# Kernel optimization log

Hardware: AMD Instinct MI355X
Metric: run time of the kernel (lower is better)

Reference implementation:

```python
import jax, jax.numpy as jnp
import numpy as np

B, N, FIN = 64, 128, 768
NFEAT, NHID, NHEADS, NCLASS = 1024, 512, 8, 512
ALPHA = 0.2
NEG_E = -9e15
NEG_S = -9e10


def setup_inputs():
    rng = np.random.RandomState(0)
    x = rng.randn(B, N, FIN).astype(np.float32)
    offset_mapping = np.zeros((B, N, 2), dtype=np.int32)
    attention_mask = np.zeros((B, N), dtype=np.float32)
    tag = np.zeros((B, N), dtype=np.float32)
    for b in range(B):
        pos, k, groups = 1, 0, 0
        n_words = int(rng.randint(30, 60))
        for _ in range(n_words):
            wl = int(rng.randint(1, 4))
            if k + wl > 120:
                break
            for _t in range(wl):
                offset_mapping[b, k] = (pos, pos + 2)  # contiguous inside word
                pos += 2
                k += 1
            pos += 1  # 1-char gap => word boundary: end == next_start - 1
            groups += 1
        groups -= 1  # last word is never closed (matches torch loop semantics)
        attention_mask[b, :groups] = 1.0
        tag[b, :groups] = (rng.rand(groups) > 0.1).astype(np.float32)
        tag[b, 0] = 1.0
    adj = (rng.rand(B, N, N) < 0.3).astype(np.float32)
    adj = np.clip(adj + np.eye(N, dtype=np.float32)[None], 0.0, 1.0)
    s = 0.02
    p = {
        'Wg_w': s * rng.randn(FIN, NFEAT), 'Wg_b': np.zeros(NFEAT),
        'hW_w': s * rng.randn(NHEADS, NFEAT, NHID), 'hW_b': np.zeros((NHEADS, NHID)),
        'ha_w': s * rng.randn(NHEADS, 2 * NHID), 'ha_b': np.zeros(NHEADS),
        'oW_w': s * rng.randn(NHID * NHEADS, NCLASS), 'oW_b': np.zeros(NCLASS),
        'oa_w': s * rng.randn(2 * NCLASS), 'oa_b': np.zeros(()),
        'fin_w': s * rng.randn(NCLASS, 1), 'fin_b': np.zeros(1),
    }
    inp = {
        'x': jnp.asarray(x), 'tag': jnp.asarray(tag),
        'offset_mapping': jnp.asarray(offset_mapping),
        'attention_mask': jnp.asarray(attention_mask), 'adj': jnp.asarray(adj),
    }
    for kk, vv in p.items():
        inp[kk] = jnp.asarray(np.asarray(vv, dtype=np.float32))
    return inp


def _group_pool(x, offs):
    # Vectorized form of the offset-grouped mean pooling loop.
    zero = (offs[:, :, 0] == 0) & (offs[:, :, 1] == 0)  # padding rows
    fz = jnp.argmax(zero, axis=1)                       # first padding row (break)
    pos = jnp.arange(N)
    valid = pos[None, :] < fz[:, None]
    nxt_start = jnp.concatenate([offs[:, 1:, 0], jnp.zeros((offs.shape[0], 1), offs.dtype)], axis=1)
    boundary = valid & (offs[:, :, 1] == nxt_start - 1)
    bi = boundary.astype(jnp.int32)
    cs = jnp.cumsum(bi, axis=1)
    seg = cs - bi                 # exclusive cumsum: group id per token
    G = cs[:, -1]                 # number of closed groups per row

    def per(xb, segb, bb):
        sums = jax.ops.segment_sum(xb, segb, num_segments=N + 1)[:N]
        cnts = jax.ops.segment_sum(jnp.ones((N,), xb.dtype), segb, num_segments=N + 1)[:N]
        ends = jax.ops.segment_sum((jnp.arange(N) + 1) * bb, segb, num_segments=N + 1)[:N]
        return sums, cnts, ends

    sums, cnts, ends = jax.vmap(per)(x, seg, bi)
    g = jnp.arange(N)[None, :]
    gv = g < G[:, None]
    x_off = jnp.where(gv[..., None], sums / jnp.maximum(cnts, 1.0)[..., None], 0.0)
    starts = jnp.concatenate([jnp.zeros((offs.shape[0], 1), jnp.int32), ends[:, :-1]], axis=1)
    starts = jnp.where(gv, starts, 0)
    ends = jnp.where(gv, ends, 0)
    return x_off, jnp.stack([starts, ends], axis=-1)  # [B,N,F_in], [B,N,2]


def _expand_row(fix):
    # Flatten [start,end) ranges in order until the first [0,0] row; rest = arange.
    zr = (fix[:, 0] == 0) & (fix[:, 1] == 0)
    fz = jnp.argmax(zr)
    valid = jnp.arange(N) < fz
    lens = jnp.where(valid, fix[:, 1] - fix[:, 0], 0)
    csum = jnp.cumsum(lens)
    excl = csum - lens
    total = csum[-1]
    l = jnp.arange(N)
    k = jnp.clip(jnp.searchsorted(csum, l, side='right'), 0, N - 1)
    val = fix[k, 0] + (l - excl[k])
    return jnp.where(l < total, val, l)


def _scores(x_off, tag, attention_mask, adj, Wg_w, Wg_b, hW_w, hW_b, ha_w, ha_b, oW_w, oW_b, oa_w, oa_b, fin_w, fin_b):
    xw = x_off @ Wg_w + Wg_b                                    # [B,N,NFEAT]
    h = jnp.einsum('bnf,hfo->bhno', xw, hW_w) + hW_b[None, :, None, :]
    # e_ij = leakyrelu(a1.h_i + a2.h_j + b): decomposition of a([h_i||h_j])
    e = jax.nn.leaky_relu(
        jnp.einsum('bhno,ho->bhn', h, ha_w[:, :NHID])[:, :, :, None]
        + jnp.einsum('bhno,ho->bhn', h, ha_w[:, NHID:])[:, :, None, :]
        + ha_b[None, :, None, None], ALPHA)
    att = jax.nn.softmax(jnp.where(adj[:, None, :, :] > 0, e, NEG_E), axis=-1)
    x1 = jax.nn.elu(jnp.einsum('bhij,bhjo->bhio', att, h))
    x1 = x1.transpose(0, 2, 1, 3).reshape(x1.shape[0], N, NHEADS * NHID)
    h2 = x1 @ oW_w + oW_b
    e2 = jax.nn.leaky_relu((h2 @ oa_w[:NCLASS])[:, :, None]
                           + (h2 @ oa_w[NCLASS:])[:, None, :] + oa_b, ALPHA)
    att2 = jax.nn.softmax(jnp.where(adj > 0, e2, NEG_E), axis=-1)
    x2 = jax.nn.elu(jnp.einsum('bij,bjo->bio', att2, h2))
    logits = (x2 @ fin_w + fin_b)[..., 0]                        # [B,N]
    m = jnp.where(tag > 0, attention_mask, 0.0)
    sc = jax.nn.softmax(jnp.where(m > 0, logits * m, NEG_S), axis=1)
    summary = m.sum(axis=1)
    ii = (jnp.arange(N, 0, -1).astype(jnp.float32)[None, :] / summary[:, None]) * m
    ii = jax.nn.softmax(jnp.where(m > 0, ii, NEG_S), axis=1)
    return sc + ii


def reference(x, tag, offset_mapping, attention_mask, adj, Wg_w, Wg_b, hW_w, hW_b, ha_w, ha_b, oW_w, oW_b, oa_w, oa_b, fin_w, fin_b):
    x_off, index_group = _group_pool(x, offset_mapping)
    sc = _scores(x_off, tag, attention_mask, adj, Wg_w, Wg_b, hW_w, hW_b, ha_w, ha_b, oW_w, oW_b, oa_w, oa_b, fin_w, fin_b)
    order = jnp.argsort(-sc, axis=1)  # jax argsort is stable; matches torch stable descending
    bidx = jnp.arange(sc.shape[0])[:, None]
    fix = index_group.at[bidx, order].set(index_group)  # scatter_(dim=1) with permutation index
    return jax.vmap(_expand_row)(fix)
```

## Files before the change

### kernel.cpp

```cpp
#include <hip/hip_runtime.h>
#include <cstddef>
#include <cstdint>

#define B_ 64
#define N_ 128
#define FIN_ 768
#define NEG_E_ (-9.0e15f)
#define NEG_S_ (-9.0e10f)
#define CHUNK_ 16

typedef unsigned short u16;
typedef unsigned int u32;
typedef float f32x4 __attribute__((ext_vector_type(4)));
typedef short s16x8 __attribute__((ext_vector_type(8)));
typedef u16 u16x4 __attribute__((ext_vector_type(4)));

__device__ __forceinline__ u16 f2bf(float x) {
  u32 u = __float_as_uint(x);
  return (u16)((u + 0x7fffu + ((u >> 16) & 1u)) >> 16);
}
__device__ __forceinline__ float b2f(u16 h) {
  return __uint_as_float(((u32)h) << 16);
}

__global__ __launch_bounds__(128) void group_pool_kernel(
    const float* __restrict__ x, const int* __restrict__ offs,
    u16* __restrict__ xoh, u16* __restrict__ xol, int* __restrict__ ig)
{
  const int b = blockIdx.x;
  const int fc = blockIdx.y;
  const int tid = threadIdx.x;
  __shared__ int o0[N_], o1[N_];
  __shared__ int bnd[N_];
  __shared__ float invlen[N_];
  __shared__ int st[N_], en[N_];
  __shared__ int Gs;
  o0[tid] = offs[(b * N_ + tid) * 2 + 0];
  o1[tid] = offs[(b * N_ + tid) * 2 + 1];
  bnd[tid] = -1;
  __syncthreads();
  if (tid == 0) {
    int fz = N_;
    for (int k = 0; k < N_; ++k) { if (o0[k] == 0 && o1[k] == 0) { fz = k; break; } }
    int g = 0, prev = 0;
    for (int k = 0; k < fz; ++k) {
      int nxt = (k + 1 < N_) ? o0[k + 1] : 0;
      if (o1[k] == nxt - 1 && g < N_) {
        bnd[k] = g;
        invlen[g] = 1.0f / (float)(k + 1 - prev);
        st[g] = prev;
        en[g] = k + 1;
        prev = k + 1;
        ++g;
      }
    }
    Gs = g;
  }
  __syncthreads();
  const int G = Gs;
  const int f = fc * 128 + tid;
  const float* xb = x + (size_t)b * N_ * FIN_ + f;
  float acc = 0.0f;
  for (int k0 = 0; k0 < N_; k0 += 8) {
    float v[8];
#pragma unroll
    for (int u = 0; u < 8; ++u) v[u] = xb[(size_t)(k0 + u) * FIN_];
#pragma unroll
    for (int u = 0; u < 8; ++u) {
      acc += v[u];
      int g = bnd[k0 + u];
      if (g >= 0) {
        float mean = acc * invlen[g];
        u16 hh = f2bf(mean);
        size_t oo = ((size_t)b * N_ + g) * FIN_ + f;
        xoh[oo] = hh;
        xol[oo] = f2bf(mean - b2f(hh));
        acc = 0.0f;
      }
    }
  }
  for (int g = G; g < N_; ++g) {
    size_t oo = ((size_t)b * N_ + g) * FIN_ + f;
    xoh[oo] = 0;
    xol[oo] = 0;
  }
  if (fc == 0) {
    int g = tid;
    ig[(b * N_ + g) * 2 + 0] = (g < G) ? st[g] : 0;
    ig[(b * N_ + g) * 2 + 1] = (g < G) ? en[g] : 0;
  }
}

__global__ __launch_bounds__(256) void pack_wgT(
    const float* __restrict__ w, u16* __restrict__ th, u16* __restrict__ tl)
{
  __shared__ float t[32][33];
  const int k0 = blockIdx.x * 32, n0 = blockIdx.y * 32;
  const int r = threadIdx.x >> 3;
  const int c = (threadIdx.x & 7) * 4;
  float4 v = *(const float4*)(w + (size_t)(k0 + r) * 1024 + n0 + c);
  t[r][c] = v.x; t[r][c + 1] = v.y; t[r][c + 2] = v.z; t[r][c + 3] = v.w;
  __syncthreads();
  u16x4 hv, lv;
#pragma unroll
  for (int i = 0; i < 4; ++i) {
    float xv = t[c + i][r];
    u16 h = f2bf(xv);
    hv[i] = h; lv[i] = f2bf(xv - b2f(h));
  }
  size_t dst = (size_t)(n0 + r) * 768 + k0 + c;
  *(u16x4*)(th + dst) = hv;
  *(u16x4*)(tl + dst) = lv;
}
__global__ __launch_bounds__(256) void pack_hwT(
    const float* __restrict__ w, u16* __restrict__ th, u16* __restrict__ tl)
{
  __shared__ float t[32][33];
  const int o0 = blockIdx.x * 32, f0 = blockIdx.y * 32, hd = blockIdx.z;
  const int r = threadIdx.x >> 3;
  const int c = (threadIdx.x & 7) * 4;
  float4 v = *(const float4*)(w + ((size_t)hd * 1024 + f0 + r) * 512 + o0 + c);
  t[r][c] = v.x; t[r][c + 1] = v.y; t[r][c + 2] = v.z; t[r][c + 3] = v.w;
  __syncthreads();
  u16x4 hv, lv;
#pragma unroll
  for (int i = 0; i < 4; ++i) {
    float xv = t[c + i][r];
    u16 h = f2bf(xv);
    hv[i] = h; lv[i] = f2bf(xv - b2f(h));
  }
  size_t dst = ((size_t)hd * 512 + o0 + r) * 1024 + f0 + c;
  *(u16x4*)(th + dst) = hv;
  *(u16x4*)(tl + dst) = lv;
}
__global__ __launch_bounds__(256) void pack_owT(
    const float* __restrict__ w, u16* __restrict__ th, u16* __restrict__ tl)
{
  __shared__ float t[32][33];
  const int k0 = blockIdx.x * 32, o0 = blockIdx.y * 32;
  const int r = threadIdx.x >> 3;
  const int c = (threadIdx.x & 7) * 4;
  float4 v = *(const float4*)(w + (size_t)(k0 + r) * 512 + o0 + c);
  t[r][c] = v.x; t[r][c + 1] = v.y; t[r][c + 2] = v.z; t[r][c + 3] = v.w;
  __syncthreads();
  u16x4 hv, lv;
#pragma unroll
  for (int i = 0; i < 4; ++i) {
    float xv = t[c + i][r];
    u16 h = f2bf(xv);
    hv[i] = h; lv[i] = f2bf(xv - b2f(h));
  }
  size_t dst = (size_t)(o0 + r) * 4096 + k0 + c;
  *(u16x4*)(th + dst) = hv;
  *(u16x4*)(tl + dst) = lv;
}

__global__ __launch_bounds__(256) void mfma_split_gemm(
    const u16* __restrict__ Ah, const u16* __restrict__ Al,
    const u16* __restrict__ Bh, const u16* __restrict__ Bl,
    const float* __restrict__ bias, int bias_mode,
    u16* __restrict__ Oh, u16* __restrict__ Ol, float* __restrict__ Of,
    int out_f32, int do_elu,
    int K, int lda, int ldb,
    long long Az, long long Bz,
    int msh, long long s_mb, int nsh, long long s_nb, long long s_n,
    long long zb_s, long long zh_s, int zH)
{
  __shared__ u16 As_h[128][40];
  __shared__ u16 As_l[128][40];
  __shared__ u16 Bs_h[128][40];
  __shared__ u16 Bs_l[128][40];
  const int tid = threadIdx.x;
  const int wave = tid >> 6, lane = tid & 63;
  const int wm = (wave >> 1) * 64, wn = (wave & 1) * 64;
  const int bn = blockIdx.x * 128, bm = blockIdx.y * 128;
  const int z = blockIdx.z;
  const u16* Ahb = Ah + (long long)z * Az;
  const u16* Alb = Al + (long long)z * Az;
  const u16* Bhb = Bh + (long long)z * Bz;
  const u16* Blb = Bl + (long long)z * Bz;
  const int lm = lane & 15, lq = lane >> 4;

  const int sr = tid >> 1;
  const int sc = (tid & 1) * 16;
  const size_t ga = (size_t)(bm + sr) * lda + sc;
  const size_t gb = (size_t)(bn + sr) * ldb + sc;

  f32x4 acc[4][4];
#pragma unroll
  for (int i = 0; i < 4; ++i)
#pragma unroll
    for (int j = 0; j < 4; ++j) acc[i][j] = (f32x4){0.0f, 0.0f, 0.0f, 0.0f};

  uint4 r0, r1, r2, r3, r4, r5, r6, r7;
  r0 = *(const uint4*)(Ahb + ga);
  r1 = *(const uint4*)(Ahb + ga + 8);
  r2 = *(const uint4*)(Alb + ga);
  r3 = *(const uint4*)(Alb + ga + 8);
  r4 = *(const uint4*)(Bhb + gb);
  r5 = *(const uint4*)(Bhb + gb + 8);
  r6 = *(const uint4*)(Blb + gb);
  r7 = *(const uint4*)(Blb + gb + 8);

  for (int k0 = 0; k0 < K; k0 += 32) {
    __syncthreads();
    *(uint4*)&As_h[sr][sc] = r0;
    *(uint4*)&As_h[sr][sc + 8] = r1;
    *(uint4*)&As_l[sr][sc] = r2;
    *(uint4*)&As_l[sr][sc + 8] = r3;
    *(uint4*)&Bs_h[sr][sc] = r4;
    *(uint4*)&Bs_h[sr][sc + 8] = r5;
    *(uint4*)&Bs_l[sr][sc] = r6;
    *(uint4*)&Bs_l[sr][sc + 8] = r7;
    __syncthreads();
    int kn = k0 + 32;
    if (kn < K) {
      r0 = *(const uint4*)(Ahb + ga + kn);
      r1 = *(const uint4*)(Ahb + ga + kn + 8);
      r2 = *(const uint4*)(Alb + ga + kn);
      r3 = *(const uint4*)(Alb + ga + kn + 8);
      r4 = *(const uint4*)(Bhb + gb + kn);
      r5 = *(const uint4*)(Bhb + gb + kn + 8);
      r6 = *(const uint4*)(Blb + gb + kn);
      r7 = *(const uint4*)(Blb + gb + kn + 8);
    }
    s16x8 fa_h[4], fa_l[4], fb_h[4], fb_l[4];
#pragma unroll
    for (int t = 0; t < 4; ++t) {
      fa_h[t] = *(const s16x8*)&As_h[wm + t * 16 + lm][lq * 8];
      fa_l[t] = *(const s16x8*)&As_l[wm + t * 16 + lm][lq * 8];
      fb_h[t] = *(const s16x8*)&Bs_h[wn + t * 16 + lm][lq * 8];
      fb_l[t] = *(const s16x8*)&Bs_l[wn + t * 16 + lm][lq * 8];
    }
#pragma unroll
    for (int i = 0; i < 4; ++i)
#pragma unroll
      for (int j = 0; j < 4; ++j) {
        acc[i][j] = __builtin_amdgcn_mfma_f32_16x16x32_bf16(fa_h[i], fb_h[j], acc[i][j], 0, 0, 0);
        acc[i][j] = __builtin_amdgcn_mfma_f32_16x16x32_bf16(fa_h[i], fb_l[j], acc[i][j], 0, 0, 0);
        acc[i][j] = __builtin_amdgcn_mfma_f32_16x16x32_bf16(fa_l[i], fb_h[j], acc[i][j], 0, 0, 0);
      }
  }

  __syncthreads();
  const long long zoff = (long long)(z / zH) * zb_s + (long long)(z % zH) * zh_s;
  const int mmask = (1 << msh) - 1;
  const int nmask = (1 << nsh) - 1;
  char* lds_raw = (char*)&As_h[0][0] + wave * 4608;
  const int rn = lane >> 2;
  const int rm = (lane & 3) * 16;

  if (out_f32) {
    float* slab = (float*)lds_raw;
#pragma unroll
    for (int j = 0; j < 4; ++j) {
#pragma unroll
      for (int i = 0; i < 4; ++i) {
        int mb = bm + wm + i * 16 + lq * 4;
        int n = bn + wn + j * 16 + lm;
        f32x4 v = acc[i][j];
        if (bias_mode == 1) v += bias[n];
        else if (bias_mode == 2) { f32x4 b4 = *(const f32x4*)&bias[mb]; v += b4; }
        if (do_elu) {
          v.x = v.x > 0.0f ? v.x : expm1f(v.x);
          v.y = v.y > 0.0f ? v.y : expm1f(v.y);
          v.z = v.z > 0.0f ? v.z : expm1f(v.z);
          v.w = v.w > 0.0f ? v.w : expm1f(v.w);
        }
        *(f32x4*)&slab[lm * 68 + i * 16 + lq * 4] = v;
      }
      __syncthreads();
      int n = bn + wn + j * 16 + rn;
      int mbase = bm + wm + rm;
      long long off = (long long)(mbase >> msh) * s_mb + (mbase & mmask)
                    + (long long)(n >> nsh) * s_nb + (long long)(n & nmask) * s_n + zoff;
      const float* src = &slab[rn * 68 + rm];
      f32x4 v0 = *(const f32x4*)(src + 0);
      f32x4 v1 = *(const f32x4*)(src + 4);
      f32x4 v2 = *(const f32x4*)(src + 8);
      f32x4 v3 = *(const f32x4*)(src + 12);
      *(f32x4*)(Of + off + 0)  = v0;
      *(f32x4*)(Of + off + 4)  = v1;
      *(f32x4*)(Of + off + 8)  = v2;
      *(f32x4*)(Of + off + 12) = v3;
      __syncthreads();
    }
  } else {
    u16* slab_h = (u16*)lds_raw;
    u16* slab_l = slab_h + 16 * 72;
#pragma unroll
    for (int j = 0; j < 4; ++j) {
#pragma unroll
      for (int i = 0; i < 4; ++i) {
        int mb = bm + wm + i * 16 + lq * 4;
        int n = bn + wn + j * 16 + lm;
        f32x4 v = acc[i][j];
        if (bias_mode == 1) v += bias[n];
        else if (bias_mode == 2) { f32x4 b4 = *(const f32x4*)&bias[mb]; v += b4; }
        if (do_elu) {
          v.x = v.x > 0.0f ? v.x : expm1f(v.x);
          v.y = v.y > 0.0f ? v.y : expm1f(v.y);
          v.z = v.z > 0.0f ? v.z : expm1f(v.z);
          v.w = v.w > 0.0f ? v.w : expm1f(v.w);
        }
        u16 h0 = f2bf(v.x), h1 = f2bf(v.y), h2 = f2bf(v.z), h3 = f2bf(v.w);
        u16x4 hv = {h0, h1, h2, h3};
        u16x4 lv = {f2bf(v.x - b2f(h0)), f2bf(v.y - b2f(h1)),
                    f2bf(v.z - b2f(h2)), f2bf(v.w - b2f(h3))};
        *(u16x4*)&slab_h[lm * 72 + i * 16 + lq * 4] = hv;
        *(u16x4*)&slab_l[lm * 72 + i * 16 + lq * 4] = lv;
      }
      __syncthreads();
      int n = bn + wn + j * 16 + rn;
      int mbase = bm + wm + rm;
      long long off = (long long)(mbase >> msh) * s_mb + (mbase & mmask)
                    + (long long)(n >> nsh) * s_nb + (long long)(n & nmask) * s_n + zoff;
      const u16* sh = &slab_h[rn * 72 + rm];
      const u16* sl = &slab_l[rn * 72 + rm];
      uint4 h0 = *(const uint4*)(sh + 0);
      uint4 h1 = *(const uint4*)(sh + 8);
      uint4 l0 = *(const uint4*)(sl + 0);
      uint4 l1 = *(const uint4*)(sl + 8);
      *(uint4*)(Oh + off + 0) = h0;
      *(uint4*)(Oh + off + 8) = h1;
      *(uint4*)(Ol + off + 0) = l0;
      *(uint4*)(Ol + off + 8) = l1;
      __syncthreads();
    }
  }
}

__global__ __launch_bounds__(256) void reduce4_bias(
    const float* __restrict__ ps, const float* __restrict__ bias,
    float* __restrict__ h2T, int col0)
{
  int base = (blockIdx.x * 256 + threadIdx.x) * 4;
  int o = base >> 11, m = base & 2047;
  f32x4 v = *(const f32x4*)(ps + base);
  v += *(const f32x4*)(ps + base + 1048576);
  v += *(const f32x4*)(ps + base + 2097152);
  v += *(const f32x4*)(ps + base + 3145728);
  v += bias[o];
  *(f32x4*)(h2T + (size_t)o * 8192 + col0 + m) = v;
}

__global__ __launch_bounds__(512) void dot_pairs_hT(
    const u16* __restrict__ hTh, const u16* __restrict__ hTl,
    const float* __restrict__ W,
    float* __restrict__ esrc, float* __restrict__ edst)
{
  int bh = blockIdx.x;
  int head = bh & 7;
  int tid = threadIdx.x;
  int os = tid >> 7, i = tid & 127;
  const u16* ph = hTh + (size_t)bh * 65536 + (size_t)os * 16384 + i;
  const u16* pl = hTl + (size_t)bh * 65536 + (size_t)os * 16384 + i;
  const float* w1 = W + head * 1024 + os * 128;
  float s1 = 0.0f, s2 = 0.0f;
#pragma unroll 8
  for (int o = 0; o < 128; ++o) {
    float hv = b2f(ph[o * 128]) + b2f(pl[o * 128]);
    s1 = fmaf(hv, w1[o], s1);
    s2 = fmaf(hv, w1[512 + o], s2);
  }
  __shared__ float sh1[4][128], sh2[4][128];
  sh1[os][i] = s1;
  sh2[os][i] = s2;
  __syncthreads();
  if (os == 0) {
    esrc[bh * 128 + i] = sh1[0][i] + sh1[1][i] + sh1[2][i] + sh1[3][i];
    edst[bh * 128 + i] = sh2[0][i] + sh2[1][i] + sh2[2][i] + sh2[3][i];
  }
}

__global__ __launch_bounds__(512) void dot_pairs_h2T(
    const float* __restrict__ h2T, const float* __restrict__ oa,
    float* __restrict__ e2s, float* __restrict__ e2d)
{
  int b = blockIdx.x;
  int tid = threadIdx.x;
  int os = tid >> 7, i = tid & 127;
  const float* hb = h2T + (size_t)os * 128 * 8192 + b * 128 + i;
  const float* oa1 = oa + os * 128;
  float s1 = 0.0f, s2 = 0.0f;
#pragma unroll 8
  for (int o = 0; o < 128; ++o) {
    float hv = hb[(size_t)o * 8192];
    s1 = fmaf(hv, oa1[o], s1);
    s2 = fmaf(hv, oa1[512 + o], s2);
  }
  __shared__ float sh1[4][128], sh2[4][128];
  sh1[os][i] = s1;
  sh2[os][i] = s2;
  __syncthreads();
  if (os == 0) {
    e2s[b * 128 + i] = sh1[0][i] + sh1[1][i] + sh1[2][i] + sh1[3][i];
    e2d[b * 128 + i] = sh2[0][i] + sh2[1][i] + sh2[2][i] + sh2[3][i];
  }
}

__global__ __launch_bounds__(64) void edge_softmax_kernel(
    const float* __restrict__ esrc, const float* __restrict__ edst,
    const float* __restrict__ bias, const float* __restrict__ adj,
    float* __restrict__ attf, u16* __restrict__ atth, u16* __restrict__ attl,
    int H, int split)
{
  int row = blockIdx.x;
  int lane = threadIdx.x;
  int i = row & 127;
  int bh = row >> 7;
  int hd = bh % H;
  int b = bh / H;
  float es = esrc[row] + bias[hd];
  const float* adjr = adj + ((size_t)b * N_ + i) * N_;
  const float* edr = edst + (size_t)bh * N_;
  float v[2];
#pragma unroll
  for (int t = 0; t < 2; ++t) {
    int j = lane + t * 64;
    float e = es + edr[j];
    e = (e >= 0.0f) ? e : 0.2f * e;
    v[t] = (adjr[j] > 0.0f) ? e : NEG_E_;
  }
  float mx = fmaxf(v[0], v[1]);
  for (int off = 32; off; off >>= 1) mx = fmaxf(mx, __shfl_xor(mx, off));
  float e0 = expf(v[0] - mx), e1 = expf(v[1] - mx);
  float sm = e0 + e1;
  for (int off = 32; off; off >>= 1) sm += __shfl_xor(sm, off);
  float inv = 1.0f / sm;
  float p0 = e0 * inv, p1 = e1 * inv;
  size_t base = (size_t)row * N_;
  if (split) {
    u16 h0 = f2bf(p0), h1 = f2bf(p1);
    atth[base + lane] = h0;
    attl[base + lane] = f2bf(p0 - b2f(h0));
    atth[base + lane + 64] = h1;
    attl[base + lane + 64] = f2bf(p1 - b2f(h1));
  } else {
    attf[base + lane] = p0;
    attf[base + lane + 64] = p1;
  }
}

__global__ __launch_bounds__(256) void bgemm_elu_bt_f32(
    const float* __restrict__ A, const float* __restrict__ BT,
    float* __restrict__ C)
{
  __shared__ float As[16][64];
  __shared__ float Bs[16][68];
  const int tid = threadIdx.x;
  const int tm = blockIdx.x >> 3, tn = blockIdx.x & 7;
  const int bm = tm * 64, bn = tn * 64;
  const int b = blockIdx.y;
  const float* Ab = A + (size_t)b * 16384;
  const float* BTb = BT + (size_t)b * 128;
  const int ty = tid >> 4, tx = tid & 15;
  const int ar = tid >> 2, ac = (tid & 3) * 4;
  float acc[4][4];
#pragma unroll
  for (int i = 0; i < 4; ++i)
#pragma unroll
    for (int j = 0; j < 4; ++j) acc[i][j] = 0.0f;

  for (int k0 = 0; k0 < 128; k0 += 16) {
    float4 av = *(const float4*)(Ab + (size_t)(bm + ar) * 128 + k0 + ac);
    float4 bv = *(const float4*)(BTb + (size_t)(bn + ar) * 8192 + k0 + ac);
    __syncthreads();
    As[ac + 0][ar] = av.x; As[ac + 1][ar] = av.y; As[ac + 2][ar] = av.z; As[ac + 3][ar] = av.w;
    Bs[ac + 0][ar] = bv.x; Bs[ac + 1][ar] = bv.y; Bs[ac + 2][ar] = bv.z; Bs[ac + 3][ar] = bv.w;
    __syncthreads();
#pragma unroll
    for (int kk = 0; kk < 16; ++kk) {
      float a[4], bb[4];
      *(float4*)a  = *(const float4*)&As[kk][ty * 4];
      *(float4*)bb = *(const float4*)&Bs[kk][tx * 4];
#pragma unroll
      for (int i = 0; i < 4; ++i)
#pragma unroll
        for (int j = 0; j < 4; ++j)
          acc[i][j] = fmaf(a[i], bb[j], acc[i][j]);
    }
  }
#pragma unroll
  for (int i = 0; i < 4; ++i) {
    int row = b * 128 + bm + ty * 4 + i;
    float4 v;
    v.x = acc[i][0] > 0.0f ? acc[i][0] : expm1f(acc[i][0]);
    v.y = acc[i][1] > 0.0f ? acc[i][1] : expm1f(acc[i][1]);
    v.z = acc[i][2] > 0.0f ? acc[i][2] : expm1f(acc[i][2]);
    v.w = acc[i][3] > 0.0f ? acc[i][3] : expm1f(acc[i][3]);
    *(float4*)(C + (size_t)row * 512 + bn + tx * 4) = v;
  }
}

__global__ __launch_bounds__(256) void logits_kernel(
    const float* __restrict__ X, const float* __restrict__ w,
    const float* __restrict__ bptr, float* __restrict__ out, int R)
{
  int wv = (blockIdx.x * 256 + threadIdx.x) >> 6;
  int lane = threadIdx.x & 63;
  if (wv >= R) return;
  const float* xr = X + (size_t)wv * 512;
  float s = 0.0f;
#pragma unroll
  for (int i = 0; i < 8; ++i) {
    int c = lane + i * 64;
    s = fmaf(xr[c], w[c], s);
  }
  for (int off = 32; off; off >>= 1) s += __shfl_down(s, off);
  if (lane == 0) out[wv] = s + bptr[0];
}

__global__ __launch_bounds__(128) void finalize_kernel(
    const float* __restrict__ logits, const float* __restrict__ tag,
    const float* __restrict__ amask, const int* __restrict__ ig,
    int* __restrict__ out)
{
  const int b = blockIdx.x, tid = threadIdx.x;
  __shared__ float red[N_];
  __shared__ float scs[N_];
  __shared__ int fs[N_], fe[N_], lens[N_], csum[N_];
  __shared__ int redi[N_];

  float lg = logits[b * N_ + tid];
  float tg = tag[b * N_ + tid];
  float am = amask[b * N_ + tid];
  float m = (tg > 0.0f) ? am : 0.0f;

  float in1 = (m > 0.0f) ? lg * m : NEG_S_;
  red[tid] = in1; __syncthreads();
  for (int s = 64; s > 0; s >>= 1) { if (tid < s) red[tid] = fmaxf(red[tid], red[tid + s]); __syncthreads(); }
  float M1 = red[0]; __syncthreads();
  float e1 = expf(in1 - M1);
  red[tid] = e1; __syncthreads();
  for (int s = 64; s > 0; s >>= 1) { if (tid < s) red[tid] += red[tid + s]; __syncthreads(); }
  float S1 = red[0]; __syncthreads();
  float sc = e1 / S1;

  red[tid] = m; __syncthreads();
  for (int s = 64; s > 0; s >>= 1) { if (tid < s) red[tid] += red[tid + s]; __syncthreads(); }
  float SM = red[0]; __syncthreads();

  float in2 = (m > 0.0f) ? ((float)(N_ - tid) / SM) * m : NEG_S_;
  red[tid] = in2; __syncthreads();
  for (int s = 64; s > 0; s >>= 1) { if (tid < s) red[tid] = fmaxf(red[tid], red[tid + s]); __syncthreads(); }
  float M2 = red[0]; __syncthreads();
  float e2 = expf(in2 - M2);
  red[tid] = e2; __syncthreads();
  for (int s = 64; s > 0; s >>= 1) { if (tid < s) red[tid] += red[tid + s]; __syncthreads(); }
  float S2 = red[0]; __syncthreads();
  float ii = e2 / S2;

  scs[tid] = sc + ii;
  __syncthreads();

  float si = scs[tid];
  int rank = 0;
  for (int j = 0; j < N_; ++j) {
    float sj = scs[j];
    rank += (sj > si) || (sj == si && j < tid);
  }
  fs[tid] = ig[(b * N_ + rank) * 2 + 0];
  fe[tid] = ig[(b * N_ + rank) * 2 + 1];
  __syncthreads();

  redi[tid] = (fs[tid] == 0 && fe[tid] == 0) ? tid : N_;
  __syncthreads();
  for (int s = 64; s > 0; s >>= 1) { if (tid < s) redi[tid] = min(redi[tid], redi[tid + s]); __syncthreads(); }
  int fz = redi[0]; __syncthreads();
  lens[tid] = (tid < fz) ? (fe[tid] - fs[tid]) : 0;
  __syncthreads();
  if (tid == 0) {
    int r = 0;
    for (int k = 0; k < N_; ++k) { r += lens[k]; csum[k] = r; }
  }
  __syncthreads();
  int total = csum[N_ - 1];
  int l = tid;
  int k = 0;
  while (k < N_ && csum[k] <= l) ++k;
  if (k > N_ - 1) k = N_ - 1;
  int val = fs[k] + (l - (csum[k] - lens[k]));
  out[b * N_ + l] = (l < total) ? val : l;
}

extern "C" void kernel_launch(void* const* d_in, const int* in_sizes, int n_in,
                              void* d_out, int out_size, void* d_ws, size_t ws_size,
                              hipStream_t stream)
{
  const float* x     = (const float*)d_in[0];
  const float* tag   = (const float*)d_in[1];
  const int*   offs  = (const int*)  d_in[2];
  const float* amask = (const float*)d_in[3];
  const float* adj   = (const float*)d_in[4];
  const float* Wg_w  = (const float*)d_in[5];
  const float* Wg_b  = (const float*)d_in[6];
  const float* hW_w  = (const float*)d_in[7];
  const float* hW_b  = (const float*)d_in[8];
  const float* ha_w  = (const float*)d_in[9];
  const float* ha_b  = (const float*)d_in[10];
  const float* oW_w  = (const float*)d_in[11];
  const float* oW_b  = (const float*)d_in[12];
  const float* oa_w  = (const float*)d_in[13];
  const float* oa_b  = (const float*)d_in[14];
  const float* fin_w = (const float*)d_in[15];
  const float* fin_b = (const float*)d_in[16];
  int* out = (int*)d_out;

  char* ws = (char*)d_ws;
  size_t o = 0;
  int* ig     = (int*)(ws + o);  o += 131072;
  u16* WgT_h  = (u16*)(ws + o);  o += 1572864;
  u16* WgT_l  = (u16*)(ws + o);  o += 1572864;
  u16* hWT_h  = (u16*)(ws + o);  o += 8388608;
  u16* hWT_l  = (u16*)(ws + o);  o += 8388608;
  u16* oWT_h  = (u16*)(ws + o);  o += 4194304;
  u16* oWT_l  = (u16*)(ws + o);  o += 4194304;
  float* h2T  = (float*)(ws + o); o += 16777216;
  float* esrc = (float*)(ws + o); o += 65536;
  float* edst = (float*)(ws + o); o += 65536;
  float* e2s  = (float*)(ws + o); o += 32768;
  float* e2d  = (float*)(ws + o); o += 32768;
  float* lgts = (float*)(ws + o); o += 32768;
  u16* xw_h   = (u16*)(ws + o);  o += 16777216;
  u16* xw_l   = (u16*)(ws + o);  o += 16777216;
  char* pool  = ws + o;          o += 75497472;

  u16* xoff_h = (u16*)(pool + 0);
  u16* xoff_l = (u16*)(pool + 12582912);
  u16* hT_h   = (u16*)(pool + 0);
  u16* hT_l   = (u16*)(pool + 16777216);
  u16* x1_h   = (u16*)(pool + 33554432);
  u16* x1_l   = (u16*)(pool + 50331648);
  u16* att_h  = (u16*)(pool + 67108864);
  u16* att_l  = (u16*)(pool + 71303168);
  float* ps   = (float*)(pool + 0);
  float* att2 = (float*)(pool + 0);
  float* x2   = (float*)(pool + 4194304);

  pack_wgT<<<dim3(24, 32), 256, 0, stream>>>(Wg_w, WgT_h, WgT_l);
  pack_hwT<<<dim3(16, 32, 8), 256, 0, stream>>>(hW_w, hWT_h, hWT_l);
  pack_owT<<<dim3(128, 16), 256, 0, stream>>>(oW_w, oWT_h, oWT_l);

  group_pool_kernel<<<dim3(B_, 6), 128, 0, stream>>>(x, offs, xoff_h, xoff_l, ig);

  mfma_split_gemm<<<dim3(64, 8, 1), 256, 0, stream>>>(
      WgT_h, WgT_l, xoff_h, xoff_l, Wg_b, 2,
      xw_h, xw_l, nullptr, 0, 0,
      768, 768, 768, 0, 0,
      10, 0, 13, 0, 1024, 0, 0, 1);

  for (int b0 = 0; b0 < B_; b0 += CHUNK_) {
    mfma_split_gemm<<<dim3(32, 16, 1), 256, 0, stream>>>(
        xw_h + (size_t)b0 * 131072, xw_l + (size_t)b0 * 131072,
        hWT_h, hWT_l, hW_b, 1,
        hT_h, hT_l, nullptr, 0, 0,
        1024, 1024, 1024, 0, 0,
        7, 524288, 9, 65536, 128, 0, 0, 1);

    dot_pairs_hT<<<CHUNK_ * 8, 512, 0, stream>>>(hT_h, hT_l, ha_w, esrc, edst);
    edge_softmax_kernel<<<CHUNK_ * 8 * 128, 64, 0, stream>>>(
        esrc, edst, ha_b, adj + (size_t)b0 * 16384, nullptr, att_h, att_l, 8, 1);

    mfma_split_gemm<<<dim3(1, 4, CHUNK_ * 8), 256, 0, stream>>>(
        hT_h, hT_l, att_h, att_l, nullptr, 0,
        x1_h, x1_l, nullptr, 0, 1,
        128, 128, 128, 65536, 16384,
        9, 0, 7, 0, 4096, 524288, 512, 8);

    mfma_split_gemm<<<dim3(4, 16, 4), 256, 0, stream>>>(
        x1_h, x1_l, oWT_h, oWT_l, nullptr, 0,
        nullptr, nullptr, ps, 1, 0,
        1024, 4096, 4096, 1024, 1024,
        13, 0, 9, 0, 2048, 0, 1048576, 4);
    reduce4_bias<<<1024, 256, 0, stream>>>(ps, oW_b, h2T, b0 * 128);
  }

  dot_pairs_h2T<<<64, 512, 0, stream>>>(h2T, oa_w, e2s, e2d);
  edge_softmax_kernel<<<8192, 64, 0, stream>>>(e2s, e2d, oa_b, adj,
      att2, nullptr, nullptr, 1, 0);
  bgemm_elu_bt_f32<<<dim3(16, 64), 256, 0, stream>>>(att2, h2T, x2);

  logits_kernel<<<2048, 256, 0, stream>>>(x2, fin_w, fin_b, lgts, 8192);
  finalize_kernel<<<B_, 128, 0, stream>>>(lgts, tag, amask, ig, out);
}
```

Before: 873.6 us.

## Add 512-thread 128x256-tile split-bf16 GEMM with triple-buffered direct-to-LDS loads

Introduces a new GEMM kernel with 8 waves, a 128x256 output tile, and a three-stage LDS ring filled by global_load_lds. Staging of the next tiles is interleaved with MFMA phases, using s_setprio and barriers to overlap loads with compute. It is used for the Wg projection and the per-head hW projection GEMMs. The aim is higher operand reuse and better latency hiding, at the cost of about 144KB of LDS per block, occupancy of likely one block per CU, and fewer blocks in the grid.

```diff
diff --git a/kernel.cpp b/kernel.cpp
--- a/kernel.cpp
+++ b/kernel.cpp
@@ -330,6 +330,155 @@
   }
 }
 
+#define G8_BUF 49152
+
+#define STAGE_A8(T) do { const int _t = (T); if (_t < nt) {                    \
+    const int _q = _t % 3;                                                     \
+    _Pragma("unroll")                                                          \
+    for (int rg_ = 0; rg_ < 2; ++rg_) {                                        \
+      const int r_ = wave * 16 + rg_ * 8 + srow;                               \
+      const u16* s_ = Asel + (size_t)(bm + r_) * lda + _t * 32 + scol;         \
+      __builtin_amdgcn_global_load_lds(                                        \
+          (const __attribute__((address_space(1))) void*)s_,                   \
+          (__attribute__((address_space(3))) void*)(ldsb + _q * G8_BUF +       \
+              (wave * 16 + rg_ * 8) * 128),                                    \
+          16, 0, 0);                                                           \
+    } } } while (0)
+
+#define STAGE_B8(T, RG0) do { const int _t = (T); if (_t < nt) {               \
+    const int _q = _t % 3;                                                     \
+    _Pragma("unroll")                                                          \
+    for (int rg_ = (RG0); rg_ < (RG0) + 2; ++rg_) {                            \
+      const int r_ = wave * 32 + rg_ * 8 + srow;                               \
+      const u16* s_ = Bsel + (size_t)(bn + r_) * ldb + _t * 32 + scol;         \
+      __builtin_amdgcn_global_load_lds(                                        \
+          (const __attribute__((address_space(1))) void*)s_,                   \
+          (__attribute__((address_space(3))) void*)(ldsb + _q * G8_BUF +       \
+              16384 + (wave * 32 + rg_ * 8) * 128),                            \
+          16, 0, 0);                                                           \
+    } } } while (0)
+
+#define GPHASE(J, STG) do {                                                    \
+    s16x8 fb0 = *(const s16x8*)(Bbase + (J) * 2048 + hbyt);                    \
+    s16x8 fb1 = *(const s16x8*)(Bbase + (J) * 2048 + lbyt);                    \
+    STG;                                                                       \
+    __builtin_amdgcn_s_barrier();                                              \
+    asm volatile("s_waitcnt lgkmcnt(0)" ::: "memory");                         \
+    __builtin_amdgcn_sched_barrier(0);                                         \
+    __builtin_amdgcn_s_setprio(1);                                             \
+    _Pragma("unroll")                                                          \
+    for (int i_ = 0; i_ < 4; ++i_) {                                           \
+      acc[i_][J] = __builtin_amdgcn_mfma_f32_16x16x32_bf16(fa[i_][0], fb0, acc[i_][J], 0, 0, 0); \
+      acc[i_][J] = __builtin_amdgcn_mfma_f32_16x16x32_bf16(fa[i_][0], fb1, acc[i_][J], 0, 0, 0); \
+      acc[i_][J] = __builtin_amdgcn_mfma_f32_16x16x32_bf16(fa[i_][1], fb0, acc[i_][J], 0, 0, 0); \
+    }                                                                          \
+    __builtin_amdgcn_s_setprio(0);                                             \
+  } while (0)
+
+__global__ __launch_bounds__(512) void mfma_split_gemm8(
+    const u16* __restrict__ Ah, const u16* __restrict__ Al,
+    const u16* __restrict__ Bh, const u16* __restrict__ Bl,
+    const float* __restrict__ bias, int bias_mode,
+    u16* __restrict__ Oh, u16* __restrict__ Ol,
+    int K, int lda, int ldb,
+    int msh, long long s_mb, int nsh, long long s_nb, long long s_n)
+{
+  __shared__ __align__(128) char ldsb[3 * G8_BUF];
+  const int tid = threadIdx.x;
+  const int wave = tid >> 6, lane = tid & 63;
+  const int wm = (wave >> 2) * 64, wn = (wave & 3) * 64;
+  const int bn = blockIdx.x * 256, bm = blockIdx.y * 128;
+  const int lm = lane & 15, lq = lane >> 4;
+  const int nt = K >> 5;
+
+  const int srow = lane >> 3;
+  const int sl = (lane & 7) ^ srow;
+  const int scol = (sl & 3) * 8;
+  const u16* Asel = (sl < 4) ? Ah : Al;
+  const u16* Bsel = (sl < 4) ? Bh : Bl;
+
+  const int hbyt = (lq ^ (lm & 7)) * 16;
+  const int lbyt = hbyt ^ 64;
+
+  f32x4 acc[4][4];
+#pragma unroll
+  for (int i = 0; i < 4; ++i)
+#pragma unroll
+    for (int j = 0; j < 4; ++j) acc[i][j] = (f32x4){0.0f, 0.0f, 0.0f, 0.0f};
+
+  STAGE_A8(0); STAGE_B8(0, 0); STAGE_B8(0, 2);
+  STAGE_A8(1); STAGE_B8(1, 0); STAGE_B8(1, 2);
+  if (nt > 1) asm volatile("s_waitcnt vmcnt(6)" ::: "memory");
+  else        asm volatile("s_waitcnt vmcnt(0)" ::: "memory");
+  __builtin_amdgcn_s_barrier();
+
+  for (int t = 0; t < nt; ++t) {
+    const int q = t % 3;
+    const char* Abase = ldsb + q * G8_BUF + (wm + lm) * 128;
+    const char* Bbase = ldsb + q * G8_BUF + 16384 + (wn + lm) * 128;
+    s16x8 fa[4][2];
+#pragma unroll
+    for (int i = 0; i < 4; ++i) {
+      fa[i][0] = *(const s16x8*)(Abase + i * 2048 + hbyt);
+      fa[i][1] = *(const s16x8*)(Abase + i * 2048 + lbyt);
+    }
+    GPHASE(0, (void)0);
+    __builtin_amdgcn_s_barrier();
+    GPHASE(1, STAGE_A8(t + 2));
+    __builtin_amdgcn_s_barrier();
+    GPHASE(2, STAGE_B8(t + 2, 0));
+    __builtin_amdgcn_s_barrier();
+    GPHASE(3, STAGE_B8(t + 2, 2));
+    if (t + 1 < nt) {
+      if (t + 2 < nt) asm volatile("s_waitcnt vmcnt(6)" ::: "memory");
+      else            asm volatile("s_waitcnt vmcnt(0)" ::: "memory");
+      __builtin_amdgcn_s_barrier();
+    }
+  }
+
+  __syncthreads();
+  const int mmask = (1 << msh) - 1;
+  const int nmask = (1 << nsh) - 1;
+  char* lds_raw = ldsb + wave * 4608;
+  const int rn = lane >> 2;
+  const int rm = (lane & 3) * 16;
+  u16* slab_h = (u16*)lds_raw;
+  u16* slab_l = slab_h + 16 * 72;
+#pragma unroll
+  for (int j = 0; j < 4; ++j) {
+#pragma unroll
+    for (int i = 0; i < 4; ++i) {
+      int mb = bm + wm + i * 16 + lq * 4;
+      int n = bn + wn + j * 16 + lm;
+      f32x4 v = acc[i][j];
+      if (bias_mode == 1) v += bias[n];
+      else if (bias_mode == 2) { f32x4 b4 = *(const f32x4*)&bias[mb]; v += b4; }
+      u16 h0 = f2bf(v.x), h1 = f2bf(v.y), h2 = f2bf(v.z), h3 = f2bf(v.w);
+      u16x4 hv = {h0, h1, h2, h3};
+      u16x4 lv = {f2bf(v.x - b2f(h0)), f2bf(v.y - b2f(h1)),
+                  f2bf(v.z - b2f(h2)), f2bf(v.w - b2f(h3))};
+      *(u16x4*)&slab_h[lm * 72 + i * 16 + lq * 4] = hv;
+      *(u16x4*)&slab_l[lm * 72 + i * 16 + lq * 4] = lv;
+    }
+    __syncthreads();
+    int n = bn + wn + j * 16 + rn;
+    int mbase = bm + wm + rm;
+    long long off = (long long)(mbase >> msh) * s_mb + (mbase & mmask)
+                  + (long long)(n >> nsh) * s_nb + (long long)(n & nmask) * s_n;
+    const u16* sh = &slab_h[rn * 72 + rm];
+    const u16* slp = &slab_l[rn * 72 + rm];
+    uint4 h0 = *(const uint4*)(sh + 0);
+    uint4 h1 = *(const uint4*)(sh + 8);
+    uint4 l0 = *(const uint4*)(slp + 0);
+    uint4 l1 = *(const uint4*)(slp + 8);
+    *(uint4*)(Oh + off + 0) = h0;
+    *(uint4*)(Oh + off + 8) = h1;
+    *(uint4*)(Ol + off + 0) = l0;
+    *(uint4*)(Ol + off + 8) = l1;
+    __syncthreads();
+  }
+}
+
 __global__ __launch_bounds__(256) void reduce4_bias(
     const float* __restrict__ ps, const float* __restrict__ bias,
     float* __restrict__ h2T, int col0)
@@ -644,19 +793,19 @@
 
   group_pool_kernel<<<dim3(B_, 6), 128, 0, stream>>>(x, offs, xoff_h, xoff_l, ig);
 
-  mfma_split_gemm<<<dim3(64, 8, 1), 256, 0, stream>>>(
+  mfma_split_gemm8<<<dim3(32, 8), 512, 0, stream>>>(
       WgT_h, WgT_l, xoff_h, xoff_l, Wg_b, 2,
-      xw_h, xw_l, nullptr, 0, 0,
-      768, 768, 768, 0, 0,
-      10, 0, 13, 0, 1024, 0, 0, 1);
+      xw_h, xw_l,
+      768, 768, 768,
+      10, 0, 13, 0, 1024);
 
   for (int b0 = 0; b0 < B_; b0 += CHUNK_) {
-    mfma_split_gemm<<<dim3(32, 16, 1), 256, 0, stream>>>(
+    mfma_split_gemm8<<<dim3(16, 16), 512, 0, stream>>>(
         xw_h + (size_t)b0 * 131072, xw_l + (size_t)b0 * 131072,
         hWT_h, hWT_l, hW_b, 1,
-        hT_h, hT_l, nullptr, 0, 0,
-        1024, 1024, 1024, 0, 0,
-        7, 524288, 9, 65536, 128, 0, 0, 1);
+        hT_h, hT_l,
+        1024, 1024, 1024,
+        7, 524288, 9, 65536, 128);
 
     dot_pairs_hT<<<CHUNK_ * 8, 512, 0, stream>>>(hT_h, hT_l, ha_w, esrc, edst);
     edge_softmax_kernel<<<CHUNK_ * 8 * 128, 64, 0, stream>>>(
```

Result: faster. 855.9 us (-2.0%).
